# Kernel tuning notes

Hardware: AMD Instinct MI355X
Metric: run time of the kernel (lower is better)

The kernel has to match this reference:

```python
import jax, jax.numpy as jnp
import numpy as np

N = 50000; FIN = 64; H = 128; E = 800000; T = 8
P = 250000; D = 500000; G = 20000; V = 2000; O = 2


def _mp(h, Ws, Wn, b, edge_src, edge_dst, n):
    # mean-aggregation message passing: relu(h Ws + mean_neigh(h) Wn + b)
    deg = jax.ops.segment_sum(jnp.ones(edge_dst.shape[0], h.dtype), edge_dst, n)
    agg = jax.ops.segment_sum(h[edge_src], edge_dst, n) / jnp.maximum(deg, 1.0)[:, None]
    return jax.nn.relu(h @ Ws + agg @ Wn + b)


def _forward(x, W_enc_self, W_enc_nei, b_enc, W2_self, W2_nei, b2, Wd1, bd1, Wd2, bd2,
             counts, edge_src, edge_dst, place_idx, src_idx, t_idx, dst_nodes, dst_seg,
             group_id, variant_of_group):
    n = x.shape[0]
    p = place_idx.shape[0]
    g = variant_of_group.shape[0]
    v = counts.shape[0]
    # first encoder, then T sequential second_encoder applications (feature generations)
    h0 = _mp(x, W_enc_self, W_enc_nei, b_enc, edge_src, edge_dst, n)

    def step(h, _):
        h2 = _mp(h, W2_self, W2_nei, b2, edge_src, edge_dst, n)
        return h2, h2

    _, hs = jax.lax.scan(step, h0, None, length=T)
    feats = jnp.concatenate([h0[None], hs], axis=0)  # [T+1, N, H]

    # gather (place, src) features at the generation index of each prediction
    place_f = feats[t_idx, place_idx]                 # [P, H]
    src_f = feats[t_idx, src_idx]                     # [P, H]
    # dst feature = sum over the destination set of each prediction
    dst_f = jax.ops.segment_sum(feats[t_idx[dst_seg], dst_nodes], dst_seg, p)  # [P, H]

    cat = jnp.concatenate([place_f, src_f, dst_f], axis=-1)  # [P, 3H]
    logits = jax.nn.relu(cat @ Wd1 + bd1) @ Wd2 + bd2        # [P, O]
    logprob = jax.nn.log_softmax(logits, axis=-1)            # [P, O]

    # prev_prob: inclusive running sum of per-step logprob sums within each variant
    group_sums = jax.ops.segment_sum(logprob, group_id, g)   # [G, O]
    cum = jnp.cumsum(group_sums, axis=0)
    var_tot = jax.ops.segment_sum(group_sums, variant_of_group, v)
    var_excl = jnp.cumsum(var_tot, axis=0) - var_tot
    within = cum - var_excl[variant_of_group]                # [G, O]
    prev = within[group_id]                                  # [P, O]

    logc = jnp.log(counts / jnp.sum(counts))                 # log(count/total) per variant
    add = logprob + prev + logc[variant_of_group[group_id]][:, None]
    return jnp.zeros((n, logits.shape[-1]), x.dtype).at[place_idx].add(add)


def setup_inputs() -> dict:
    ks = jax.random.split(jax.random.key(0), 24)
    s = jnp.float32(0.05)
    f32 = jnp.float32
    i32 = jnp.int32
    return {
        "x": jax.random.normal(ks[0], (N, FIN), f32),
        "W_enc_self": jax.random.normal(ks[1], (FIN, H), f32) * s,
        "W_enc_nei": jax.random.normal(ks[2], (FIN, H), f32) * s,
        "b_enc": jax.random.normal(ks[3], (H,), f32) * s,
        "W2_self": jax.random.normal(ks[4], (H, H), f32) * s,
        "W2_nei": jax.random.normal(ks[5], (H, H), f32) * s,
        "b2": jax.random.normal(ks[6], (H,), f32) * s,
        "Wd1": jax.random.normal(ks[7], (3 * H, 3 * H), f32) * s,
        "bd1": jax.random.normal(ks[8], (3 * H,), f32) * s,
        "Wd2": jax.random.normal(ks[9], (3 * H, O), f32) * s,
        "bd2": jax.random.normal(ks[10], (O,), f32) * s,
        "counts": jax.random.uniform(ks[11], (V,), f32) + 0.5,
        "edge_src": jax.random.randint(ks[12], (E,), 0, N, i32),
        "edge_dst": jax.random.randint(ks[13], (E,), 0, N, i32),
        "place_idx": jax.random.randint(ks[14], (P,), 0, N, i32),
        "src_idx": jax.random.randint(ks[15], (P,), 0, N, i32),
        "t_idx": jax.random.randint(ks[16], (P,), 0, T + 1, i32),
        "dst_nodes": jax.random.randint(ks[17], (D,), 0, N, i32),
        "dst_seg": jnp.sort(jax.random.randint(ks[18], (D,), 0, P, i32)),
        "group_id": jnp.sort(jax.random.randint(ks[19], (P,), 0, G, i32)),
        "variant_of_group": jnp.sort(jax.random.randint(ks[20], (G,), 0, V, i32)),
    }


def reference(x, W_enc_self, W_enc_nei, b_enc, W2_self, W2_nei, b2, Wd1, bd1, Wd2, bd2,
              counts, edge_src, edge_dst, place_idx, src_idx, t_idx, dst_nodes, dst_seg,
              group_id, variant_of_group):
    return _forward(x, W_enc_self, W_enc_nei, b_enc, W2_self, W2_nei, b2, Wd1, bd1, Wd2, bd2,
                    counts, edge_src, edge_dst, place_idx, src_idx, t_idx, dst_nodes, dst_seg,
                    group_id, variant_of_group)
```

## Files before the change

kernel.cpp:

```cpp
#include <hip/hip_runtime.h>
#include <math.h>

#define NN 50000
#define FINN 64
#define HD 128
#define EE 800000
#define TT 8
#define PP 250000
#define DD 500000
#define GG 20000
#define VV 2000
#define OO 2

#define DEC_GRID 256
#define DEC_TILES ((PP + 63) / 64)

typedef short short8 __attribute__((ext_vector_type(8)));
typedef float f32x4 __attribute__((ext_vector_type(4)));

__device__ __forceinline__ unsigned short f2bf(float f) {
    unsigned int u = __float_as_uint(f);
    u += 0x7fffu + ((u >> 16) & 1u);
    return (unsigned short)(u >> 16);
}
__device__ __forceinline__ float bf2f(unsigned short u) {
    return __uint_as_float(((unsigned int)u) << 16);
}

struct us8 { unsigned short v[8]; };

__device__ __forceinline__ void gload_lds16(const void* g, void* l) {
    __builtin_amdgcn_global_load_lds((__attribute__((address_space(1))) void*)g,
                                     (__attribute__((address_space(3))) void*)l, 16, 0, 0);
}

__global__ void count_k(const int* __restrict__ idx, int* __restrict__ counts, int n) {
    int i = blockIdx.x * blockDim.x + threadIdx.x;
    if (i < n) atomicAdd(&counts[idx[i]], 1);
}

__global__ void blk_sum_k(const int* __restrict__ counts, int n, int* __restrict__ bsum) {
    __shared__ int buf[256];
    int t = threadIdx.x, i = blockIdx.x * 256 + t;
    buf[t] = (i < n) ? counts[i] : 0;
    __syncthreads();
    for (int off = 128; off > 0; off >>= 1) {
        if (t < off) buf[t] += buf[t + off];
        __syncthreads();
    }
    if (t == 0) bsum[blockIdx.x] = buf[0];
}

__global__ void scan_small_k(const int* __restrict__ bsum, int nb, int* __restrict__ boff) {
    __shared__ int buf[256];
    int t = threadIdx.x;
    int v = (t < nb) ? bsum[t] : 0;
    buf[t] = v;
    __syncthreads();
    for (int off = 1; off < 256; off <<= 1) {
        int u = (t >= off) ? buf[t - off] : 0;
        __syncthreads();
        buf[t] += u;
        __syncthreads();
    }
    if (t < nb) boff[t] = buf[t] - v;
}

__global__ void rowptr_fill_k(const int* __restrict__ counts, const int* __restrict__ boff,
                              int n, int* __restrict__ rowptr, int total) {
    __shared__ int buf[256];
    int t = threadIdx.x, i = blockIdx.x * 256 + t;
    int v = (i < n) ? counts[i] : 0;
    buf[t] = v;
    __syncthreads();
    for (int off = 1; off < 256; off <<= 1) {
        int u = (t >= off) ? buf[t - off] : 0;
        __syncthreads();
        buf[t] += u;
        __syncthreads();
    }
    if (i < n) rowptr[i] = boff[blockIdx.x] + buf[t] - v;
    if (i == 0) rowptr[n] = total;
}

__global__ void lb_rowptr_k(const int* __restrict__ arr, int n, int* __restrict__ rowptr, int m) {
    int i = blockIdx.x * blockDim.x + threadIdx.x;
    if (i > m) return;
    int lo = 0, hi = n;
    while (lo < hi) {
        int mid = (lo + hi) >> 1;
        if (arr[mid] < i) lo = mid + 1; else hi = mid;
    }
    rowptr[i] = lo;
}

__global__ void fill_csr_k(const int* __restrict__ esrc, const int* __restrict__ edst,
                           const int* __restrict__ rowptr, int* __restrict__ cursor,
                           int* __restrict__ outi, int n) {
    int e = blockIdx.x * blockDim.x + threadIdx.x;
    if (e < n) {
        int d = edst[e];
        int pos = atomicAdd(&cursor[d], 1);
        outi[rowptr[d] + pos] = esrc[e];
    }
}

__global__ void hist9_k(const int* __restrict__ t_idx, int* __restrict__ hist) {
    __shared__ int l[9];
    if (threadIdx.x < 9) l[threadIdx.x] = 0;
    __syncthreads();
    int p = blockIdx.x * 256 + threadIdx.x;
    if (p < PP) atomicAdd(&l[t_idx[p]], 1);
    __syncthreads();
    if (threadIdx.x < 9) atomicAdd(&hist[threadIdx.x], l[threadIdx.x]);
}

__global__ void scan9_k(const int* __restrict__ hist, int* __restrict__ boff9) {
    if (threadIdx.x == 0) {
        int a = 0;
        for (int i = 0; i < 9; ++i) { boff9[i] = a; a += hist[i]; }
    }
}

__global__ void bucket_perm_k(const int* __restrict__ t_idx, const int* __restrict__ boff9,
                              int* __restrict__ cursor9, int* __restrict__ pperm) {
    __shared__ int lcnt[9];
    __shared__ int lbase[9];
    int tid = threadIdx.x;
    int p = blockIdx.x * 256 + tid;
    if (tid < 9) lcnt[tid] = 0;
    __syncthreads();
    int t = 0, lr = 0;
    bool ok = p < PP;
    if (ok) {
        t = t_idx[p];
        lr = atomicAdd(&lcnt[t], 1);
    }
    __syncthreads();
    if (tid < 9) lbase[tid] = atomicAdd(&cursor9[tid], lcnt[tid]);
    __syncthreads();
    if (ok) pperm[boff9[t] + lbase[t] + lr] = p;
}

__global__ void prep_k(const float* __restrict__ x,
                       const float* __restrict__ Wes, const float* __restrict__ Wen,
                       const float* __restrict__ W2s, const float* __restrict__ W2n,
                       const float* __restrict__ Wd1,
                       unsigned short* __restrict__ xb, unsigned short* __restrict__ wenc_t,
                       unsigned short* __restrict__ w2_t, unsigned short* __restrict__ wd1t) {
    int i = blockIdx.x * 256 + threadIdx.x;
    if (i < NN * FINN) xb[i] = f2bf(x[i]);
    if (i < HD * 2 * FINN) {
        int c = i / (2 * FINN), k = i - c * (2 * FINN);
        wenc_t[i] = f2bf((k < FINN) ? Wes[k * HD + c] : Wen[(k - FINN) * HD + c]);
    }
    if (i < HD * 2 * HD) {
        int c = i / (2 * HD), k = i - c * (2 * HD);
        w2_t[i] = f2bf((k < HD) ? W2s[k * HD + c] : W2n[(k - HD) * HD + c]);
    }
    if (i < 384 * 384) {
        int n = i / 384, k = i - n * 384;
        wd1t[i] = f2bf(Wd1[k * 384 + n]);
    }
}

template <int KIN>
__launch_bounds__(256)
__global__ void mpf_k(const unsigned short* __restrict__ hin,
                      const int* __restrict__ rowptr, const int* __restrict__ csr_src,
                      const unsigned short* __restrict__ Wt, const float* __restrict__ bias,
                      unsigned short* __restrict__ hout) {
    constexpr int CPL = KIN / 64;
    __shared__ unsigned short sm[32 * KIN];
    int tid = threadIdx.x;
    int r = tid >> 3;
    int sl = tid & 7;
    int node = blockIdx.x * 32 + r;
    int rx = r & 7;

    if (node < NN) {
        int s = rowptr[node], e = rowptr[node + 1];
        float acc[8 * CPL] = {};
        int i = s, iB = s + 1;
        int srcA = (i < e) ? csr_src[i] : 0;
        int srcB = (iB < e) ? csr_src[iB] : 0;
        while (i < e) {
            bool hB = iB < e;
            us8 vA0, vA1, vB0, vB1;
            vA0 = *(const us8*)&hin[(size_t)srcA * KIN + sl * (8 * CPL)];
            if constexpr (CPL == 2) vA1 = *(const us8*)&hin[(size_t)srcA * KIN + sl * 16 + 8];
            if (hB) {
                vB0 = *(const us8*)&hin[(size_t)srcB * KIN + sl * (8 * CPL)];
                if constexpr (CPL == 2) vB1 = *(const us8*)&hin[(size_t)srcB * KIN + sl * 16 + 8];
            }
            int iN = i + 2, iN2 = i + 3;
            srcA = (iN < e) ? csr_src[iN] : 0;
            srcB = (iN2 < e) ? csr_src[iN2] : 0;
#pragma unroll
            for (int j = 0; j < 8; ++j) acc[j] += bf2f(vA0.v[j]);
            if constexpr (CPL == 2)
#pragma unroll
                for (int j = 0; j < 8; ++j) acc[8 + j] += bf2f(vA1.v[j]);
            if (hB) {
#pragma unroll
                for (int j = 0; j < 8; ++j) acc[j] += bf2f(vB0.v[j]);
                if constexpr (CPL == 2)
#pragma unroll
                    for (int j = 0; j < 8; ++j) acc[8 + j] += bf2f(vB1.v[j]);
            }
            i = iN; iB = iN2;
        }
        float d = fmaxf((float)(e - s), 1.f);
        us8 o0, o1;
#pragma unroll
        for (int j = 0; j < 8; ++j) o0.v[j] = f2bf(acc[j] / d);
        int c0 = sl * CPL;
        *(us8*)&sm[r * KIN + ((c0 ^ rx) * 8)] = o0;
        if constexpr (CPL == 2) {
#pragma unroll
            for (int j = 0; j < 8; ++j) o1.v[j] = f2bf(acc[8 + j] / d);
            *(us8*)&sm[r * KIN + (((c0 + 1) ^ rx) * 8)] = o1;
        }
    }
    __syncthreads();

    int lane = tid & 63, w = tid >> 6;
    int cc = lane & 15, gq = lane >> 4;
    constexpr int K = 2 * KIN;
    int rloc = (w & 1) * 16 + cc;
    int rowA = blockIdx.x * 32 + rloc;
    bool rowok = rowA < NN;
    const unsigned short* hrow = hin + (size_t)rowA * KIN;
    int ch = (w >> 1) * 64;
    int rlx = rloc & 7;

    f32x4 acc2[4];
#pragma unroll
    for (int t = 0; t < 4; ++t) acc2[t] = (f32x4){0.f, 0.f, 0.f, 0.f};

#pragma unroll
    for (int k0 = 0; k0 < K; k0 += 32) {
        int k = k0 + gq * 8;
        short8 a = {0, 0, 0, 0, 0, 0, 0, 0};
        if (rowok) {
            if (k0 < KIN) a = *(const short8*)(hrow + k);
            else {
                int chunk = (k - KIN) >> 3;
                a = *(const short8*)&sm[rloc * KIN + ((chunk ^ rlx) * 8)];
            }
        }
#pragma unroll
        for (int t = 0; t < 4; ++t) {
            short8 b = *(const short8*)&Wt[(size_t)(ch + t * 16 + cc) * K + k];
            acc2[t] = __builtin_amdgcn_mfma_f32_16x16x32_bf16(a, b, acc2[t], 0, 0, 0);
        }
    }
#pragma unroll
    for (int t = 0; t < 4; ++t) {
        int col = ch + t * 16 + cc;
        float b1 = bias[col];
#pragma unroll
        for (int rj = 0; rj < 4; ++rj) {
            int grow = blockIdx.x * 32 + (w & 1) * 16 + gq * 4 + rj;
            if (grow < NN)
                hout[(size_t)grow * HD + col] = f2bf(fmaxf(acc2[t][rj] + b1, 0.f));
        }
    }
}

__launch_bounds__(256)
__global__ void dst_sum2_k(const unsigned short* __restrict__ feats,
                           const int* __restrict__ t_idx, const int* __restrict__ dst_nodes,
                           const int* __restrict__ dst_rowptr, const int* __restrict__ pperm,
                           unsigned short* __restrict__ dstc) {
    int tid = threadIdx.x;
    int grp = tid >> 4;
    int fl = tid & 15;
    int pi = blockIdx.x * 16 + grp;
    if (pi >= PP) return;
    int p = pperm[pi];
    long t = t_idx[p];
    const unsigned short* base = feats + t * (long)NN * HD;
    int s = dst_rowptr[p], e = dst_rowptr[p + 1];
    float acc[8] = {};
    int i = s;
    int n0 = (i < e) ? dst_nodes[i] : 0;
    int n1 = (i + 1 < e) ? dst_nodes[i + 1] : 0;
    while (i < e) {
        bool h1 = (i + 1) < e;
        us8 v0 = *(const us8*)&base[(size_t)n0 * HD + fl * 8];
        us8 v1;
        if (h1) v1 = *(const us8*)&base[(size_t)n1 * HD + fl * 8];
        int i2 = i + 2, i3 = i + 3;
        n0 = (i2 < e) ? dst_nodes[i2] : 0;
        n1 = (i3 < e) ? dst_nodes[i3] : 0;
#pragma unroll
        for (int j = 0; j < 8; ++j) acc[j] += bf2f(v0.v[j]);
        if (h1) {
#pragma unroll
            for (int j = 0; j < 8; ++j) acc[j] += bf2f(v1.v[j]);
        }
        i = i2;
    }
    us8 o;
#pragma unroll
    for (int j = 0; j < 8; ++j) o.v[j] = f2bf(acc[j]);
    *(us8*)&dstc[(size_t)pi * HD + fl * 8] = o;
}

__launch_bounds__(512, 2)
__global__ void dec6_k(const unsigned short* __restrict__ feats,
                       const unsigned short* __restrict__ dstc,
                       const int* __restrict__ place_idx, const int* __restrict__ src_idx,
                       const int* __restrict__ t_idx, const int* __restrict__ group_id,
                       const int* __restrict__ pperm,
                       const unsigned short* __restrict__ Wd1t,
                       const float* __restrict__ bd1, const float* __restrict__ Wd2,
                       const float* __restrict__ bd2, float* __restrict__ logprob,
                       float* __restrict__ group_sums) {
    __shared__ unsigned short buf[3][192 * 128];
    __shared__ unsigned int rb[3][192];
    __shared__ float lpart[3][8][64][2];

    int tid = threadIdx.x;
    int lane = tid & 63, w = tid >> 6;
    int cc = lane & 15, gq = lane >> 4;
    int bid = blockIdx.x;

    int row = min(tid, 191);
    int sec = row >> 6, pl = row & 63;
    const int* nptr = (sec == 0) ? place_idx : src_idx;
    unsigned int dstc_off = (unsigned int)((const char*)dstc - (const char*)feats);

    int nt = (DEC_TILES - 1 - bid) / DEC_GRID + 1;
    float b20 = bd2[0], b21 = bd2[1];

    if (tid < 192) {
#pragma unroll
        for (int s3 = 0; s3 < 3; ++s3) {
            int pic = min((bid + s3 * DEC_GRID) * 64 + pl, PP - 1);
            int p = pperm[pic];
            rb[s3][tid] = (sec == 2) ? (dstc_off + (unsigned int)pic * 256u)
                                     : (unsigned int)(((unsigned)t_idx[p] * NN + (unsigned)nptr[p]) * 256u);
        }
    }
    int p3 = pperm[min((bid + 3 * DEC_GRID) * 64 + pl, PP - 1)];
    int tOld = t_idx[p3], nOld = nptr[p3];
    int pCur = pperm[min((bid + 4 * DEC_GRID) * 64 + pl, PP - 1)];
    int opPP = 0, opP = 0, ogP = 0;

    short8 breg[36];
    float b1r[3], w0r[3], w1r[3];
    {
        const unsigned short* bbase = Wd1t + ((long)(w * 48 + cc) * 384 + gq * 8);
#pragma unroll
        for (int kk = 0; kk < 12; ++kk)
#pragma unroll
            for (int t = 0; t < 3; ++t)
                breg[kk * 3 + t] = *(const short8*)(bbase + (long)t * 16 * 384 + kk * 32);
#pragma unroll
        for (int t = 0; t < 3; ++t) {
            int col = w * 48 + t * 16 + cc;
            b1r[t] = bd1[col];
            w0r[t] = Wd2[col * 2 + 0];
            w1r[t] = Wd2[col * 2 + 1];
        }
    }
    __syncthreads();

    int rsub = lane >> 4, chunk = lane & 15;

#define STAGE(slot_)                                                                 \
    {                                                                                \
        _Pragma("unroll")                                                            \
        for (int i = 0; i < 6; ++i) {                                                \
            int r = w * 24 + i * 4 + rsub;                                           \
            const char* src = (const char*)feats + rb[slot_][r] +                    \
                              ((unsigned)(chunk ^ (r & 7)) << 4);                    \
            gload_lds16(src, &buf[slot_][(w * 24 + i * 4) * 128]);                   \
        }                                                                            \
    }

#define OUTPUT(tile_, slot_, opv_, ogv_)                                             \
    {                                                                                \
        int pi = (bid + (tile_) * DEC_GRID) * 64 + w * 16 + cc;                      \
        if (pi < PP) {                                                               \
            float l0 = b20, l1 = b21;                                                \
            _Pragma("unroll")                                                        \
            for (int w2 = 0; w2 < 8; ++w2) {                                         \
                l0 += lpart[slot_][w2][w * 16 + cc][0];                              \
                l1 += lpart[slot_][w2][w * 16 + cc][1];                              \
            }                                                                        \
            float mm = fmaxf(l0, l1);                                                \
            float lse = mm + logf(expf(l0 - mm) + expf(l1 - mm));                    \
            float lp0 = l0 - lse, lp1 = l1 - lse;                                    \
            logprob[(opv_)*2 + 0] = lp0;                                             \
            logprob[(opv_)*2 + 1] = lp1;                                             \
            atomicAdd(&group_sums[(ogv_)*2 + 0], lp0);                               \
            atomicAdd(&group_sums[(ogv_)*2 + 1], lp1);                               \
        }                                                                            \
    }

    STAGE(0);
    STAGE(1);

    for (int k = 0; k < nt; ++k) {
        int slot = k % 3;

        int opN = pperm[min((bid + k * DEC_GRID) * 64 + (w & 3) * 16 + cc, PP - 1)];
        int ogN = group_id[opP];
        int pNew = pperm[min((bid + (k + 5) * DEC_GRID) * 64 + pl, PP - 1)];
        int tNew = t_idx[pCur];
        int nNew = nptr[pCur];
        __builtin_amdgcn_sched_barrier(0);

        if (k + 2 < nt) STAGE((k + 2) % 3);
        __builtin_amdgcn_sched_barrier(0);

        if (k + 2 < nt) {
            if (k >= 2) { asm volatile("s_waitcnt vmcnt(21)" ::: "memory"); }
            else        { asm volatile("s_waitcnt vmcnt(17)" ::: "memory"); }
        } else if (k + 1 < nt) {
            asm volatile("s_waitcnt vmcnt(15)" ::: "memory");
        } else {
            asm volatile("s_waitcnt vmcnt(5)" ::: "memory");
        }
        __builtin_amdgcn_s_barrier();
        __builtin_amdgcn_sched_barrier(0);

        if (k >= 2 && w < 4 && lane < 16) OUTPUT(k - 2, (k - 2) % 3, opPP, ogP);

        {
            const unsigned short* bufc = &buf[slot][0];
            f32x4 acc[4][3];
#pragma unroll
            for (int s = 0; s < 4; ++s)
#pragma unroll
                for (int t = 0; t < 3; ++t) acc[s][t] = (f32x4){0.f, 0.f, 0.f, 0.f};

#pragma unroll
            for (int kk = 0; kk < 12; ++kk) {
                int seck = kk >> 2;
                int cbase = (kk & 3) * 4 + gq;
                int coff = (cbase ^ (cc & 7)) * 8;
                short8 a_c[4];
#pragma unroll
                for (int s = 0; s < 4; ++s) {
                    int lrow = seck * 64 + s * 16 + cc;
                    a_c[s] = *(const short8*)&bufc[lrow * 128 + coff];
                }
#pragma unroll
                for (int t = 0; t < 3; ++t)
#pragma unroll
                    for (int s = 0; s < 4; ++s)
                        acc[s][t] = __builtin_amdgcn_mfma_f32_16x16x32_bf16(
                            a_c[s], breg[kk * 3 + t], acc[s][t], 0, 0, 0);
            }

            float part[4][4][2] = {};
#pragma unroll
            for (int t = 0; t < 3; ++t) {
#pragma unroll
                for (int s = 0; s < 4; ++s)
#pragma unroll
                    for (int r = 0; r < 4; ++r) {
                        float h = fmaxf(acc[s][t][r] + b1r[t], 0.f);
                        part[s][r][0] += h * w0r[t];
                        part[s][r][1] += h * w1r[t];
                    }
            }
#pragma unroll
            for (int m = 1; m < 16; m <<= 1)
#pragma unroll
                for (int s = 0; s < 4; ++s)
#pragma unroll
                    for (int r = 0; r < 4; ++r) {
                        part[s][r][0] += __shfl_xor(part[s][r][0], m);
                        part[s][r][1] += __shfl_xor(part[s][r][1], m);
                    }
            if (cc == 0) {
#pragma unroll
                for (int s = 0; s < 4; ++s)
#pragma unroll
                    for (int r = 0; r < 4; ++r) {
                        int orow = s * 16 + gq * 4 + r;
                        lpart[slot][w][orow][0] = part[s][r][0];
                        lpart[slot][w][orow][1] = part[s][r][1];
                    }
            }
        }

        if (tid < 192) {
            int picw = min((bid + (k + 3) * DEC_GRID) * 64 + pl, PP - 1);
            rb[(k + 3) % 3][tid] = (sec == 2)
                ? (dstc_off + (unsigned int)picw * 256u)
                : (unsigned int)(((unsigned)tOld * NN + (unsigned)nOld) * 256u);
        }
        tOld = tNew; nOld = nNew; pCur = pNew;
        opPP = opP; opP = opN; ogP = ogN;

        asm volatile("s_waitcnt lgkmcnt(0)" ::: "memory");
        __builtin_amdgcn_s_barrier();
        __builtin_amdgcn_sched_barrier(0);
    }

    if (w < 4 && lane < 16) {
        OUTPUT(nt - 2, (nt - 2) % 3, opPP, ogP);
        int ogLast = group_id[opP];
        OUTPUT(nt - 1, (nt - 1) % 3, opP, ogLast);
    }
#undef STAGE
#undef OUTPUT
}

__global__ void within_total_k(const float* __restrict__ group_sums,
                               const int* __restrict__ var_rowptr,
                               const float* __restrict__ counts,
                               float* __restrict__ within, float* __restrict__ total) {
    __shared__ float buf[256];
    int tid = threadIdx.x;
    float s = 0.f;
    for (int i = tid; i < VV; i += 256) s += counts[i];
    buf[tid] = s;
    __syncthreads();
    for (int off = 128; off > 0; off >>= 1) {
        if (tid < off) buf[tid] += buf[tid + off];
        __syncthreads();
    }
    if (tid == 0) total[0] = buf[0];
    for (int v = tid; v < VV; v += 256) {
        int gs = var_rowptr[v], ge = var_rowptr[v + 1];
        float r0 = 0.f, r1 = 0.f;
        for (int g = gs; g < ge; ++g) {
            r0 += group_sums[2 * g + 0];
            r1 += group_sums[2 * g + 1];
            within[2 * g + 0] = r0;
            within[2 * g + 1] = r1;
        }
    }
}

__global__ void final_k(const float* __restrict__ logprob, const float* __restrict__ within,
                        const int* __restrict__ group_id, const int* __restrict__ vog,
                        const float* __restrict__ counts, const float* __restrict__ total,
                        const int* __restrict__ place_idx, float* __restrict__ outp) {
    int p = blockIdx.x * blockDim.x + threadIdx.x;
    if (p >= PP) return;
    int g = group_id[p];
    int v = vog[g];
    float lc = logf(counts[v]) - logf(total[0]);
    int node = place_idx[p];
    atomicAdd(&outp[node * 2 + 0], logprob[p * 2 + 0] + within[g * 2 + 0] + lc);
    atomicAdd(&outp[node * 2 + 1], logprob[p * 2 + 1] + within[g * 2 + 1] + lc);
}

extern "C" void kernel_launch(void* const* d_in, const int* in_sizes, int n_in,
                              void* d_out, int out_size, void* d_ws, size_t ws_size,
                              hipStream_t stream) {
    const float* x          = (const float*)d_in[0];
    const float* W_enc_self = (const float*)d_in[1];
    const float* W_enc_nei  = (const float*)d_in[2];
    const float* b_enc      = (const float*)d_in[3];
    const float* W2_self    = (const float*)d_in[4];
    const float* W2_nei     = (const float*)d_in[5];
    const float* b2         = (const float*)d_in[6];
    const float* Wd1        = (const float*)d_in[7];
    const float* bd1        = (const float*)d_in[8];
    const float* Wd2        = (const float*)d_in[9];
    const float* bd2        = (const float*)d_in[10];
    const float* counts     = (const float*)d_in[11];
    const int* edge_src     = (const int*)d_in[12];
    const int* edge_dst     = (const int*)d_in[13];
    const int* place_idx    = (const int*)d_in[14];
    const int* src_idx      = (const int*)d_in[15];
    const int* t_idx        = (const int*)d_in[16];
    const int* dst_nodes    = (const int*)d_in[17];
    const int* dst_seg      = (const int*)d_in[18];
    const int* group_id     = (const int*)d_in[19];
    const int* variant_of_group = (const int*)d_in[20];
    float* outp = (float*)d_out;

    const int NB = (NN + 255) / 256;

    unsigned short* feats = (unsigned short*)d_ws;
    unsigned short* aggb  = feats + (size_t)(TT + 1) * NN * HD;
    unsigned short* xb    = aggb + (size_t)NN * HD;
    unsigned short* dstc  = xb + (size_t)NN * FINN;
    unsigned short* wenc_t = dstc + (size_t)PP * HD;
    unsigned short* w2_t   = wenc_t + HD * 2 * FINN;
    unsigned short* wd1t   = w2_t + HD * 2 * HD;
    int* zr = (int*)(wd1t + 384 * 384);
    int* csr_counts   = zr;
    int* csr_cursor   = csr_counts + NN;
    float* group_sums = (float*)(csr_cursor + NN);
    int* hist9        = (int*)(group_sums + 2 * GG);
    int* cursor9      = hist9 + 9;
    size_t zero_words = (size_t)NN + NN + 2 * GG + 18;
    int* bsum       = cursor9 + 9;
    int* boff       = bsum + 256;
    int* boff9      = boff + 256;
    int* csr_rowptr = boff9 + 16;
    int* dst_rowptr = csr_rowptr + (NN + 1);
    int* var_rowptr = dst_rowptr + (PP + 1);
    int* csr_src    = var_rowptr + (VV + 1);
    int* pperm      = csr_src + EE;
    float* logprob  = (float*)(pperm + PP);
    float* within   = logprob + 2 * PP;
    float* total_counts = within + 2 * GG;

    hipMemsetAsync(zr, 0, zero_words * 4, stream);
    hipMemsetAsync(d_out, 0, (size_t)out_size * sizeof(float), stream);

    prep_k<<<(NN * FINN + 255) / 256, 256, 0, stream>>>(x, W_enc_self, W_enc_nei, W2_self,
                                                        W2_nei, Wd1, xb, wenc_t, w2_t, wd1t);
    count_k<<<(EE + 255) / 256, 256, 0, stream>>>(edge_dst, csr_counts, EE);
    blk_sum_k<<<NB, 256, 0, stream>>>(csr_counts, NN, bsum);
    scan_small_k<<<1, 256, 0, stream>>>(bsum, NB, boff);
    rowptr_fill_k<<<NB, 256, 0, stream>>>(csr_counts, boff, NN, csr_rowptr, EE);
    fill_csr_k<<<(EE + 255) / 256, 256, 0, stream>>>(edge_src, edge_dst, csr_rowptr,
                                                     csr_cursor, csr_src, EE);
    lb_rowptr_k<<<(PP + 256) / 256, 256, 0, stream>>>(dst_seg, DD, dst_rowptr, PP);
    lb_rowptr_k<<<(VV + 256) / 256, 256, 0, stream>>>(variant_of_group, GG, var_rowptr, VV);
    hist9_k<<<(PP + 255) / 256, 256, 0, stream>>>(t_idx, hist9);
    scan9_k<<<1, 64, 0, stream>>>(hist9, boff9);
    bucket_perm_k<<<(PP + 255) / 256, 256, 0, stream>>>(t_idx, boff9, cursor9, pperm);

    const int NB32 = (NN + 31) / 32;
    for (int r = 0; r <= TT; ++r) {
        const unsigned short* hin = (r == 0) ? xb : feats + (size_t)(r - 1) * NN * HD;
        unsigned short* hout = feats + (size_t)r * NN * HD;
        if (r == 0)
            mpf_k<FINN><<<NB32, 256, 0, stream>>>(hin, csr_rowptr, csr_src, wenc_t, b_enc, hout);
        else
            mpf_k<HD><<<NB32, 256, 0, stream>>>(hin, csr_rowptr, csr_src, w2_t, b2, hout);
    }

    dst_sum2_k<<<(PP + 15) / 16, 256, 0, stream>>>(feats, t_idx, dst_nodes, dst_rowptr, pperm, dstc);
    dec6_k<<<DEC_GRID, 512, 0, stream>>>(feats, dstc, place_idx, src_idx, t_idx,
                                         group_id, pperm, wd1t, bd1, Wd2, bd2,
                                         logprob, group_sums);

    within_total_k<<<1, 256, 0, stream>>>(group_sums, var_rowptr, counts, within, total_counts);
    final_k<<<(PP + 255) / 256, 256, 0, stream>>>(logprob, within, group_id, variant_of_group,
                                                  counts, total_counts, place_idx, outp);
}
```

Measured before the change: 989.7 us.

## Store per-generation features in 8-bit float for decoder and destination gathers

The message-passing kernel now also writes each generation's output as a custom 8-bit float (e4m3-like), while the bf16 copy only goes to two ping-pong buffers used for the recurrence. The destination-sum and decoder kernels gather these 8-bit features and dequantize them to bf16 before accumulating or feeding MFMA. This halves the bytes moved by the random gathers and the LDS staging. The cost is extra quantize/dequantize ALU work and a loss of precision in the decoder inputs, which may push outputs past the tolerance. The decoder wait counts and the partial-sum reduction are also restructured to match.

```diff
diff --git a/kernel.cpp b/kernel.cpp
--- a/kernel.cpp
+++ b/kernel.cpp
@@ -27,6 +27,32 @@
     return __uint_as_float(((unsigned int)u) << 16);
 }
 
+__device__ __forceinline__ unsigned char q8(float f) {
+    unsigned short u = f2bf(f);
+    unsigned int e = (u >> 7) & 0xffu;
+    unsigned int s = (u >> 8) & 0x80u;
+    if (e < 121u) return (unsigned char)s;
+    unsigned int m = u & 0x7fu;
+    unsigned int m3 = m >> 4, rr = m & 0xfu;
+    m3 += (rr > 8u) || (rr == 8u && (m3 & 1u));
+    unsigned int ee = e - 120u;
+    if (m3 == 8u) { m3 = 0u; ++ee; }
+    if (ee > 15u || (ee == 15u && m3 == 7u)) { ee = 15u; m3 = 6u; }
+    return (unsigned char)(s | (ee << 3) | m3);
+}
+__device__ __forceinline__ unsigned int dq1(unsigned int b) {
+    unsigned int t = b & 0x7fu;
+    unsigned int r = ((b & 0x80u) << 8) | ((t << 4) + 0x3C00u);
+    return t ? r : 0u;
+}
+__device__ __forceinline__ short8 dq8(unsigned long long v) {
+    short8 o;
+#pragma unroll
+    for (int j = 0; j < 8; ++j)
+        o[j] = (short)dq1((unsigned int)(v >> (8 * j)) & 0xffu);
+    return o;
+}
+
 struct us8 { unsigned short v[8]; };
 
 __device__ __forceinline__ void gload_lds16(const void* g, void* l) {
@@ -119,6 +145,7 @@
     if (threadIdx.x == 0) {
         int a = 0;
         for (int i = 0; i < 9; ++i) { boff9[i] = a; a += hist[i]; }
+        boff9[9] = a;
     }
 }
 
@@ -169,7 +196,7 @@
 __global__ void mpf_k(const unsigned short* __restrict__ hin,
                       const int* __restrict__ rowptr, const int* __restrict__ csr_src,
                       const unsigned short* __restrict__ Wt, const float* __restrict__ bias,
-                      unsigned short* __restrict__ hout) {
+                      unsigned short* __restrict__ hout, unsigned char* __restrict__ houtq) {
     constexpr int CPL = KIN / 64;
     __shared__ unsigned short sm[32 * KIN];
     int tid = threadIdx.x;
@@ -262,17 +289,20 @@
 #pragma unroll
         for (int rj = 0; rj < 4; ++rj) {
             int grow = blockIdx.x * 32 + (w & 1) * 16 + gq * 4 + rj;
-            if (grow < NN)
-                hout[(size_t)grow * HD + col] = f2bf(fmaxf(acc2[t][rj] + b1, 0.f));
+            if (grow < NN) {
+                float v = fmaxf(acc2[t][rj] + b1, 0.f);
+                hout[(size_t)grow * HD + col] = f2bf(v);
+                houtq[(size_t)grow * HD + col] = q8(v);
+            }
         }
     }
 }
 
 __launch_bounds__(256)
-__global__ void dst_sum2_k(const unsigned short* __restrict__ feats,
-                           const int* __restrict__ t_idx, const int* __restrict__ dst_nodes,
-                           const int* __restrict__ dst_rowptr, const int* __restrict__ pperm,
-                           unsigned short* __restrict__ dstc) {
+__global__ void dst_sum2q_k(const unsigned char* __restrict__ featsq,
+                            const int* __restrict__ t_idx, const int* __restrict__ dst_nodes,
+                            const int* __restrict__ dst_rowptr, const int* __restrict__ pperm,
+                            unsigned char* __restrict__ dstcq) {
     int tid = threadIdx.x;
     int grp = tid >> 4;
     int fl = tid & 15;
@@ -280,7 +310,7 @@
     if (pi >= PP) return;
     int p = pperm[pi];
     long t = t_idx[p];
-    const unsigned short* base = feats + t * (long)NN * HD;
+    const unsigned char* base = featsq + (size_t)t * NN * HD;
     int s = dst_rowptr[p], e = dst_rowptr[p + 1];
     float acc[8] = {};
     int i = s;
@@ -288,37 +318,40 @@
     int n1 = (i + 1 < e) ? dst_nodes[i + 1] : 0;
     while (i < e) {
         bool h1 = (i + 1) < e;
-        us8 v0 = *(const us8*)&base[(size_t)n0 * HD + fl * 8];
-        us8 v1;
-        if (h1) v1 = *(const us8*)&base[(size_t)n1 * HD + fl * 8];
+        unsigned long long v0 = *(const unsigned long long*)&base[(size_t)n0 * HD + fl * 8];
+        unsigned long long v1 = 0;
+        if (h1) v1 = *(const unsigned long long*)&base[(size_t)n1 * HD + fl * 8];
         int i2 = i + 2, i3 = i + 3;
         n0 = (i2 < e) ? dst_nodes[i2] : 0;
         n1 = (i3 < e) ? dst_nodes[i3] : 0;
 #pragma unroll
-        for (int j = 0; j < 8; ++j) acc[j] += bf2f(v0.v[j]);
+        for (int j = 0; j < 8; ++j)
+            acc[j] += bf2f((unsigned short)dq1((unsigned int)(v0 >> (8 * j)) & 0xffu));
         if (h1) {
 #pragma unroll
-            for (int j = 0; j < 8; ++j) acc[j] += bf2f(v1.v[j]);
+            for (int j = 0; j < 8; ++j)
+                acc[j] += bf2f((unsigned short)dq1((unsigned int)(v1 >> (8 * j)) & 0xffu));
         }
         i = i2;
     }
-    us8 o;
-#pragma unroll
-    for (int j = 0; j < 8; ++j) o.v[j] = f2bf(acc[j]);
-    *(us8*)&dstc[(size_t)pi * HD + fl * 8] = o;
-}
-
-__launch_bounds__(512, 2)
-__global__ void dec6_k(const unsigned short* __restrict__ feats,
-                       const unsigned short* __restrict__ dstc,
-                       const int* __restrict__ place_idx, const int* __restrict__ src_idx,
-                       const int* __restrict__ t_idx, const int* __restrict__ group_id,
-                       const int* __restrict__ pperm,
-                       const unsigned short* __restrict__ Wd1t,
-                       const float* __restrict__ bd1, const float* __restrict__ Wd2,
-                       const float* __restrict__ bd2, float* __restrict__ logprob,
-                       float* __restrict__ group_sums) {
-    __shared__ unsigned short buf[3][192 * 128];
+    unsigned long long ov = 0;
+#pragma unroll
+    for (int j = 0; j < 8; ++j) ov |= (unsigned long long)q8(acc[j]) << (8 * j);
+    *(unsigned long long*)&dstcq[(size_t)pi * HD + fl * 8] = ov;
+}
+
+__global__ void
+__attribute__((amdgpu_flat_work_group_size(512, 512), amdgpu_waves_per_eu(2, 2)))
+dec9_k(const unsigned char* __restrict__ featsq,
+       const unsigned char* __restrict__ dstcq,
+       const int* __restrict__ place_idx, const int* __restrict__ src_idx,
+       const int* __restrict__ t_idx, const int* __restrict__ group_id,
+       const int* __restrict__ pperm,
+       const unsigned short* __restrict__ Wd1t,
+       const float* __restrict__ bd1, const float* __restrict__ Wd2,
+       const float* __restrict__ bd2, float* __restrict__ logprob,
+       float* __restrict__ group_sums) {
+    __shared__ unsigned char buf[3][192 * 128];
     __shared__ unsigned int rb[3][192];
     __shared__ float lpart[3][8][64][2];
 
@@ -330,7 +363,7 @@
     int row = min(tid, 191);
     int sec = row >> 6, pl = row & 63;
     const int* nptr = (sec == 0) ? place_idx : src_idx;
-    unsigned int dstc_off = (unsigned int)((const char*)dstc - (const char*)feats);
+    unsigned int dstc_off = (unsigned int)(dstcq - featsq);
 
     int nt = (DEC_TILES - 1 - bid) / DEC_GRID + 1;
     float b20 = bd2[0], b21 = bd2[1];
@@ -340,8 +373,8 @@
         for (int s3 = 0; s3 < 3; ++s3) {
             int pic = min((bid + s3 * DEC_GRID) * 64 + pl, PP - 1);
             int p = pperm[pic];
-            rb[s3][tid] = (sec == 2) ? (dstc_off + (unsigned int)pic * 256u)
-                                     : (unsigned int)(((unsigned)t_idx[p] * NN + (unsigned)nptr[p]) * 256u);
+            rb[s3][tid] = (sec == 2) ? (dstc_off + (unsigned int)pic * 128u)
+                                     : (unsigned int)(((unsigned)t_idx[p] * NN + (unsigned)nptr[p]) * 128u);
         }
     }
     int p3 = pperm[min((bid + 3 * DEC_GRID) * 64 + pl, PP - 1)];
@@ -368,16 +401,16 @@
     }
     __syncthreads();
 
-    int rsub = lane >> 4, chunk = lane & 15;
+    int rsub8 = lane >> 3, chunk8 = lane & 7;
 
 #define STAGE(slot_)                                                                 \
     {                                                                                \
         _Pragma("unroll")                                                            \
-        for (int i = 0; i < 6; ++i) {                                                \
-            int r = w * 24 + i * 4 + rsub;                                           \
-            const char* src = (const char*)feats + rb[slot_][r] +                    \
-                              ((unsigned)(chunk ^ (r & 7)) << 4);                    \
-            gload_lds16(src, &buf[slot_][(w * 24 + i * 4) * 128]);                   \
+        for (int i = 0; i < 3; ++i) {                                                \
+            int r = w * 24 + i * 8 + rsub8;                                          \
+            const unsigned char* src = featsq + rb[slot_][r] +                       \
+                                       ((unsigned)(chunk8 ^ (r & 7)) << 4);          \
+            gload_lds16(src, &buf[slot_][(w * 24 + i * 8) * 128]);                   \
         }                                                                            \
     }
 
@@ -418,10 +451,10 @@
         __builtin_amdgcn_sched_barrier(0);
 
         if (k + 2 < nt) {
-            if (k >= 2) { asm volatile("s_waitcnt vmcnt(21)" ::: "memory"); }
-            else        { asm volatile("s_waitcnt vmcnt(17)" ::: "memory"); }
+            if (k >= 2) { asm volatile("s_waitcnt vmcnt(16)" ::: "memory"); }
+            else        { asm volatile("s_waitcnt vmcnt(11)" ::: "memory"); }
         } else if (k + 1 < nt) {
-            asm volatile("s_waitcnt vmcnt(15)" ::: "memory");
+            asm volatile("s_waitcnt vmcnt(13)" ::: "memory");
         } else {
             asm volatile("s_waitcnt vmcnt(5)" ::: "memory");
         }
@@ -431,7 +464,7 @@
         if (k >= 2 && w < 4 && lane < 16) OUTPUT(k - 2, (k - 2) % 3, opPP, ogP);
 
         {
-            const unsigned short* bufc = &buf[slot][0];
+            const unsigned char* bufc = &buf[slot][0];
             f32x4 acc[4][3];
 #pragma unroll
             for (int s = 0; s < 4; ++s)
@@ -441,13 +474,15 @@
 #pragma unroll
             for (int kk = 0; kk < 12; ++kk) {
                 int seck = kk >> 2;
-                int cbase = (kk & 3) * 4 + gq;
-                int coff = (cbase ^ (cc & 7)) * 8;
+                int eb = (kk & 3) * 32 + gq * 8;
+                int c16 = eb >> 4, sub = (eb >> 3) & 1;
                 short8 a_c[4];
 #pragma unroll
                 for (int s = 0; s < 4; ++s) {
                     int lrow = seck * 64 + s * 16 + cc;
-                    a_c[s] = *(const short8*)&bufc[lrow * 128 + coff];
+                    unsigned long long v = *(const unsigned long long*)
+                        &bufc[lrow * 128 + ((c16 ^ (lrow & 7)) << 4) + sub * 8];
+                    a_c[s] = dq8(v);
                 }
 #pragma unroll
                 for (int t = 0; t < 3; ++t)
@@ -457,44 +492,43 @@
                             a_c[s], breg[kk * 3 + t], acc[s][t], 0, 0, 0);
             }
 
-            float part[4][4][2] = {};
-#pragma unroll
-            for (int t = 0; t < 3; ++t) {
-#pragma unroll
-                for (int s = 0; s < 4; ++s)
+#pragma unroll
+            for (int s = 0; s < 4; ++s) {
+                float p0[4], p1[4];
+#pragma unroll
+                for (int r = 0; r < 4; ++r) { p0[r] = 0.f; p1[r] = 0.f; }
+#pragma unroll
+                for (int t = 0; t < 3; ++t) {
 #pragma unroll
                     for (int r = 0; r < 4; ++r) {
                         float h = fmaxf(acc[s][t][r] + b1r[t], 0.f);
-                        part[s][r][0] += h * w0r[t];
-                        part[s][r][1] += h * w1r[t];
+                        p0[r] += h * w0r[t];
+                        p1[r] += h * w1r[t];
                     }
-            }
-#pragma unroll
-            for (int m = 1; m < 16; m <<= 1)
-#pragma unroll
-                for (int s = 0; s < 4; ++s)
+                }
+#pragma unroll
+                for (int m = 1; m < 16; m <<= 1)
 #pragma unroll
                     for (int r = 0; r < 4; ++r) {
-                        part[s][r][0] += __shfl_xor(part[s][r][0], m);
-                        part[s][r][1] += __shfl_xor(part[s][r][1], m);
+                        p0[r] += __shfl_xor(p0[r], m);
+                        p1[r] += __shfl_xor(p1[r], m);
                     }
-            if (cc == 0) {
-#pragma unroll
-                for (int s = 0; s < 4; ++s)
+                if (cc == 0) {
 #pragma unroll
                     for (int r = 0; r < 4; ++r) {
                         int orow = s * 16 + gq * 4 + r;
-                        lpart[slot][w][orow][0] = part[s][r][0];
-                        lpart[slot][w][orow][1] = part[s][r][1];
+                        lpart[slot][w][orow][0] = p0[r];
+                        lpart[slot][w][orow][1] = p1[r];
                     }
+                }
             }
         }
 
         if (tid < 192) {
             int picw = min((bid + (k + 3) * DEC_GRID) * 64 + pl, PP - 1);
             rb[(k + 3) % 3][tid] = (sec == 2)
-                ? (dstc_off + (unsigned int)picw * 256u)
-                : (unsigned int)(((unsigned)tOld * NN + (unsigned)nOld) * 256u);
+                ? (dstc_off + (unsigned int)picw * 128u)
+                : (unsigned int)(((unsigned)tOld * NN + (unsigned)nOld) * 128u);
         }
         tOld = tNew; nOld = nNew; pCur = pNew;
         opPP = opP; opP = opN; ogP = ogN;
@@ -582,11 +616,12 @@
 
     const int NB = (NN + 255) / 256;
 
-    unsigned short* feats = (unsigned short*)d_ws;
-    unsigned short* aggb  = feats + (size_t)(TT + 1) * NN * HD;
-    unsigned short* xb    = aggb + (size_t)NN * HD;
-    unsigned short* dstc  = xb + (size_t)NN * FINN;
-    unsigned short* wenc_t = dstc + (size_t)PP * HD;
+    unsigned short* rot0 = (unsigned short*)d_ws;
+    unsigned short* rot1 = rot0 + (size_t)NN * HD;
+    unsigned short* xb   = rot1 + (size_t)NN * HD;
+    unsigned char* featsq = (unsigned char*)(xb + (size_t)NN * FINN);
+    unsigned char* dstcq  = featsq + (size_t)(TT + 1) * NN * HD;
+    unsigned short* wenc_t = (unsigned short*)(dstcq + (size_t)PP * HD);
     unsigned short* w2_t   = wenc_t + HD * 2 * FINN;
     unsigned short* wd1t   = w2_t + HD * 2 * HD;
     int* zr = (int*)(wd1t + 384 * 384);
@@ -627,16 +662,20 @@
 
     const int NB32 = (NN + 31) / 32;
     for (int r = 0; r <= TT; ++r) {
-        const unsigned short* hin = (r == 0) ? xb : feats + (size_t)(r - 1) * NN * HD;
-        unsigned short* hout = feats + (size_t)r * NN * HD;
+        const unsigned short* hin = (r == 0) ? xb : ((r & 1) ? rot0 : rot1);
+        unsigned short* hout = (r & 1) ? rot1 : rot0;
+        unsigned char* houtq = featsq + (size_t)r * NN * HD;
         if (r == 0)
-            mpf_k<FINN><<<NB32, 256, 0, stream>>>(hin, csr_rowptr, csr_src, wenc_t, b_enc, hout);
+            mpf_k<FINN><<<NB32, 256, 0, stream>>>(hin, csr_rowptr, csr_src, wenc_t, b_enc,
+                                                  hout, houtq);
         else
-            mpf_k<HD><<<NB32, 256, 0, stream>>>(hin, csr_rowptr, csr_src, w2_t, b2, hout);
-    }
-
-    dst_sum2_k<<<(PP + 15) / 16, 256, 0, stream>>>(feats, t_idx, dst_nodes, dst_rowptr, pperm, dstc);
-    dec6_k<<<DEC_GRID, 512, 0, stream>>>(feats, dstc, place_idx, src_idx, t_idx,
+            mpf_k<HD><<<NB32, 256, 0, stream>>>(hin, csr_rowptr, csr_src, w2_t, b2,
+                                                hout, houtq);
+    }
+
+    dst_sum2q_k<<<(PP + 15) / 16, 256, 0, stream>>>(featsq, t_idx, dst_nodes, dst_rowptr,
+                                                    pperm, dstcq);
+    dec9_k<<<DEC_GRID, 512, 0, stream>>>(featsq, dstcq, place_idx, src_idx, t_idx,
                                          group_id, pperm, wd1t, bd1, Wd2, bd2,
                                          logprob, group_sums);
 
```

Result: slower. 1.132 ms (+14.4%).
